# Kernel optimization log

Hardware: AMD Instinct MI355X
Metric: run time of the kernel (lower is better)

Reference implementation:

```python
import jax, jax.numpy as jnp
import numpy as np

K = 20            # top-k snippets selected per video
P = 0.1           # dropout prob applied to the selection mask
BATCH = 32        # number of normal videos (first half); abnormal is second half


def setup_inputs() -> dict:
    key = jax.random.key(0)
    k1, k2, k3, k4 = jax.random.split(key, 4)
    bs, t, f = 64, 2048, 1024
    features = jax.random.normal(k1, (bs, t, f), dtype=jnp.float32)
    scores = jax.random.uniform(k2, (bs, t, 1), dtype=jnp.float32)
    mask_u_abn = jax.random.uniform(k3, (BATCH, t), dtype=jnp.float32)
    mask_u_nor = jax.random.uniform(k4, (BATCH, t), dtype=jnp.float32)
    return {"features": features, "scores": scores,
            "mask_u_abn": mask_u_abn, "mask_u_nor": mask_u_nor}


def _select(feat, sc, mag, mask_u):
    # dropout on a ones tensor == Bernoulli(1-P) mask scaled by 1/(1-P)
    drop = (mask_u > P).astype(mag.dtype) / (1.0 - P)
    _, idx = jax.lax.top_k(mag * drop, K)            # [n, K] indices into t
    sel_feat = jnp.take_along_axis(feat, idx[:, :, None], axis=1)   # [n, K, f]
    sel_score = jnp.take_along_axis(sc, idx[:, :, None], axis=1)    # [n, K, 1]
    return jnp.mean(sel_score, axis=1), sel_feat     # [n,1], [n,K,f]


def reference(features, scores, mask_u_abn, mask_u_nor):
    # features: [bs, t, f], scores: [bs, t, 1]
    mags = jnp.linalg.norm(features, axis=2)         # [bs, t] L2 feature magnitudes
    nfeat, afeat = features[:BATCH], features[BATCH:]
    nsc, asc = scores[:BATCH], scores[BATCH:]
    nmag, amag = mags[:BATCH], mags[BATCH:]

    score_abnormal, abn_feamagnitude = _select(afeat, asc, amag, mask_u_abn)
    score_normal, nor_feamagnitude = _select(nfeat, nsc, nmag, mask_u_nor)
    return (score_abnormal, score_normal, abn_feamagnitude, nor_feamagnitude)
```

## Files before the change

### kernel.cpp

```cpp
#include <hip/hip_runtime.h>

#define T       2048
#define FEAT    1024
#define BTOT    64
#define BHALF   32
#define KSEL    20

__global__ __launch_bounds__(256) void mag_key_kernel(
        const float* __restrict__ feat,
        const float* __restrict__ mask_abn,
        const float* __restrict__ mask_nor,
        float* __restrict__ keys)
{
#pragma clang fp contract(off)
    const int wid  = threadIdx.x >> 6;
    const int lane = threadIdx.x & 63;
    const int row  = blockIdx.x * 4 + wid;

    __shared__ float sh[4 * 1056];
    float* lds = sh + wid * 1056;

    const float4* __restrict__ src = (const float4*)(feat + (size_t)row * FEAT);
#pragma unroll
    for (int it = 0; it < 4; ++it) {
        int f = it * 64 + lane;
        float4 v = src[f];
        int d = f * 4 + 4 * (f >> 5);
        *(float4*)(lds + d) = v;
    }
    __syncthreads();

    const int B = lane >> 3;
    const int j = lane & 7;
    const int base = B * 132 + j;

    float v0 = lds[base];
    float acc = v0 * v0;
#pragma unroll
    for (int i = 1; i < 16; ++i) {
        float w = lds[base + 8 * i];
        float p = w * w;
        acc = acc + p;
    }
    acc = acc + __shfl_xor(acc, 1);
    acc = acc + __shfl_xor(acc, 2);
    acc = acc + __shfl_xor(acc, 4);
    acc = acc + __shfl_xor(acc, 8);
    acc = acc + __shfl_xor(acc, 16);
    acc = acc + __shfl_xor(acc, 32);

    if (lane == 0) {
        float mag = sqrtf(acc);
        int b = row >> 11;
        int t = row & (T - 1);
        float m = (b < BHALF) ? mask_nor[b * T + t]
                              : mask_abn[(b - BHALF) * T + t];
        float key = (m > 0.1f) ? (mag * (1.0f / 0.9f)) : 0.0f;
        keys[row] = key;
    }
}

__global__ __launch_bounds__(256) void topk_kernel(
        const float* __restrict__ keys,
        const float* __restrict__ scores,
        int* __restrict__ sel_idx,
        float* __restrict__ out)
{
#pragma clang fp contract(off)
    const int b    = blockIdx.x;
    const int tid  = threadIdx.x;
    const int lane = tid & 63;
    const int wid  = tid >> 6;

    __shared__ unsigned long long wmax[2][4];
    __shared__ int s_sel[KSEL];

    unsigned long long p[8];
#pragma unroll
    for (int s = 0; s < 8; ++s) {
        int i = tid + 256 * s;
        float v = keys[b * T + i];
        p[s] = ((unsigned long long)__float_as_uint(v) << 32) |
               (unsigned long long)(0xFFFFFFFFu - (unsigned)i);
    }

    int sel_local[KSEL];

    for (int k = 0; k < KSEL; ++k) {
        unsigned long long best = 0ull;
#pragma unroll
        for (int s = 0; s < 8; ++s)
            if (p[s] > best) best = p[s];
#pragma unroll
        for (int d = 1; d < 64; d <<= 1) {
            unsigned long long o = __shfl_xor(best, d);
            if (o > best) best = o;
        }
        if (lane == 0) wmax[k & 1][wid] = best;
        __syncthreads();
        unsigned long long g = wmax[k & 1][0];
#pragma unroll
        for (int w = 1; w < 4; ++w)
            if (wmax[k & 1][w] > g) g = wmax[k & 1][w];
        int idx = (int)(0xFFFFFFFFu - (unsigned)(g & 0xFFFFFFFFull));
        sel_local[k] = idx;
        if ((idx & 255) == tid) p[idx >> 8] = 0ull;
    }

    if (tid == 0) {
        float a[KSEL];
        for (int k = 0; k < KSEL; ++k) a[k] = scores[b * T + sel_local[k]];
        float r[8];
        for (int jj = 0; jj < 8; ++jj) r[jj] = a[jj];
        for (int jj = 0; jj < 8; ++jj) r[jj] = r[jj] + a[8 + jj];
        float res = ((r[0] + r[1]) + (r[2] + r[3])) + ((r[4] + r[5]) + (r[6] + r[7]));
        res = res + a[16];
        res = res + a[17];
        res = res + a[18];
        res = res + a[19];
        float mean = res / 20.0f;
        int o = (b >= BHALF) ? (b - BHALF) : (BHALF + b);
        out[o] = mean;
    }
    if (tid < KSEL) sel_idx[b * KSEL + tid] = sel_local[tid];
}

__global__ __launch_bounds__(256) void gather_kernel(
        const float* __restrict__ feat,
        const int* __restrict__ sel_idx,
        float* __restrict__ out)
{
    const int k = blockIdx.x;
    const int b = blockIdx.y;
    const int t = sel_idx[b * KSEL + k];
    const float4* __restrict__ src =
        (const float4*)(feat + ((size_t)b * T + (size_t)t) * FEAT);
    size_t off;
    if (b >= BHALF) {
        off = 64 + ((size_t)(b - BHALF) * KSEL + k) * FEAT;
    } else {
        off = 64 + (size_t)BHALF * KSEL * FEAT + ((size_t)b * KSEL + k) * FEAT;
    }
    float4* __restrict__ dst = (float4*)(out + off);
    dst[threadIdx.x] = src[threadIdx.x];
}

extern "C" void kernel_launch(void* const* d_in, const int* in_sizes, int n_in,
                              void* d_out, int out_size, void* d_ws, size_t ws_size,
                              hipStream_t stream)
{
    const float* feat   = (const float*)d_in[0];
    const float* scores = (const float*)d_in[1];
    const float* mabn   = (const float*)d_in[2];
    const float* mnor   = (const float*)d_in[3];
    float* out = (float*)d_out;

    float* keys = (float*)d_ws;
    int*   sel  = (int*)((char*)d_ws + (size_t)BTOT * T * sizeof(float));

    mag_key_kernel<<<(BTOT * T) / 4, 256, 0, stream>>>(feat, mabn, mnor, keys);
    topk_kernel<<<BTOT, 256, 0, stream>>>(keys, scores, sel, out);
    gather_kernel<<<dim3(KSEL, BTOT), 256, 0, stream>>>(feat, sel, out);
}
```

Before: 686.4 us.

## Make magnitude kernel persistent with double-buffered direct global-to-LDS loads

```diff
diff --git a/kernel.cpp b/kernel.cpp
--- a/kernel.cpp
+++ b/kernel.cpp
@@ -5,64 +5,82 @@
 #define BTOT    64
 #define BHALF   32
 #define KSEL    20
+#define NROWS   (BTOT * T)
+#define MAG_BLOCKS 1280
+#define MAG_WAVES  (MAG_BLOCKS * 4)
 
-__global__ __launch_bounds__(256) void mag_key_kernel(
+__global__ __launch_bounds__(256) void mag_kernel(
         const float* __restrict__ feat,
-        const float* __restrict__ mask_abn,
-        const float* __restrict__ mask_nor,
         float* __restrict__ keys)
 {
 #pragma clang fp contract(off)
     const int wid  = threadIdx.x >> 6;
     const int lane = threadIdx.x & 63;
-    const int row  = blockIdx.x * 4 + wid;
+    const int gw   = blockIdx.x * 4 + wid;
 
-    __shared__ float sh[4 * 1056];
-    float* lds = sh + wid * 1056;
+    __shared__ float sh[4 * 2048];
+    float* buf = sh + wid * 2048;
 
-    const float4* __restrict__ src = (const float4*)(feat + (size_t)row * FEAT);
+    const int B    = lane >> 3;
+    const int j    = lane & 7;
+    const int base = B * 128 + j;
+    const int bl8  = lane & 24;
+
+    auto stage = [&](int row, float* dst) {
+        const float4* src4 = (const float4*)(feat + (size_t)row * FEAT);
 #pragma unroll
-    for (int it = 0; it < 4; ++it) {
-        int f = it * 64 + lane;
-        float4 v = src[f];
-        int d = f * 4 + 4 * (f >> 5);
-        *(float4*)(lds + d) = v;
-    }
-    __syncthreads();
+        for (int it = 0; it < 4; ++it) {
+            int q  = it * 64 + lane;
+            int qg = q ^ (((q >> 5) & 3) << 1);
+            __builtin_amdgcn_global_load_lds(
+                (const __attribute__((address_space(1))) void*)(src4 + qg),
+                (__attribute__((address_space(3))) void*)(dst + it * 256),
+                16, 0, 0);
+        }
+    };
 
-    const int B = lane >> 3;
-    const int j = lane & 7;
-    const int base = B * 132 + j;
+    int r = gw;
+    if (r < NROWS) stage(r, buf);
+    int cur = 0;
+    while (r < NROWS) {
+        const int rn = r + MAG_WAVES;
+        if (rn < NROWS) {
+            stage(rn, buf + ((cur ^ 1) << 10));
+            asm volatile("s_waitcnt vmcnt(4)" ::: "memory");
+        } else {
+            asm volatile("s_waitcnt vmcnt(0)" ::: "memory");
+        }
 
-    float v0 = lds[base];
-    float acc = v0 * v0;
+        const float* lds = buf + (cur << 10);
+
+        float w0  = lds[base + bl8];
+        float acc = w0 * w0;
 #pragma unroll
-    for (int i = 1; i < 16; ++i) {
-        float w = lds[base + 8 * i];
-        float p = w * w;
-        acc = acc + p;
-    }
-    acc = acc + __shfl_xor(acc, 1);
-    acc = acc + __shfl_xor(acc, 2);
-    acc = acc + __shfl_xor(acc, 4);
-    acc = acc + __shfl_xor(acc, 8);
-    acc = acc + __shfl_xor(acc, 16);
-    acc = acc + __shfl_xor(acc, 32);
+        for (int i = 1; i < 16; ++i) {
+            float w = lds[base + ((8 * i) ^ bl8)];
+            float p = w * w;
+            acc = acc + p;
+        }
+        acc = acc + __shfl_xor(acc, 1);
+        acc = acc + __shfl_xor(acc, 2);
+        acc = acc + __shfl_xor(acc, 4);
+        acc = acc + __shfl_xor(acc, 8);
+        acc = acc + __shfl_xor(acc, 16);
+        acc = acc + __shfl_xor(acc, 32);
 
-    if (lane == 0) {
-        float mag = sqrtf(acc);
-        int b = row >> 11;
-        int t = row & (T - 1);
-        float m = (b < BHALF) ? mask_nor[b * T + t]
-                              : mask_abn[(b - BHALF) * T + t];
-        float key = (m > 0.1f) ? (mag * (1.0f / 0.9f)) : 0.0f;
-        keys[row] = key;
+        if (lane == 0) keys[r] = sqrtf(acc);
+
+        asm volatile("s_waitcnt lgkmcnt(0)" ::: "memory");
+        cur ^= 1;
+        r = rn;
     }
 }
 
 __global__ __launch_bounds__(256) void topk_kernel(
         const float* __restrict__ keys,
         const float* __restrict__ scores,
+        const float* __restrict__ mask_abn,
+        const float* __restrict__ mask_nor,
         int* __restrict__ sel_idx,
         float* __restrict__ out)
 {
@@ -73,14 +91,16 @@
     const int wid  = tid >> 6;
 
     __shared__ unsigned long long wmax[2][4];
-    __shared__ int s_sel[KSEL];
 
     unsigned long long p[8];
 #pragma unroll
     for (int s = 0; s < 8; ++s) {
         int i = tid + 256 * s;
         float v = keys[b * T + i];
-        p[s] = ((unsigned long long)__float_as_uint(v) << 32) |
+        float m = (b < BHALF) ? mask_nor[b * T + i]
+                              : mask_abn[(b - BHALF) * T + i];
+        float key = (m > 0.1f) ? (v * (1.0f / 0.9f)) : 0.0f;
+        p[s] = ((unsigned long long)__float_as_uint(key) << 32) |
                (unsigned long long)(0xFFFFFFFFu - (unsigned)i);
     }
 
@@ -158,7 +178,7 @@
     float* keys = (float*)d_ws;
     int*   sel  = (int*)((char*)d_ws + (size_t)BTOT * T * sizeof(float));
 
-    mag_key_kernel<<<(BTOT * T) / 4, 256, 0, stream>>>(feat, mabn, mnor, keys);
-    topk_kernel<<<BTOT, 256, 0, stream>>>(keys, scores, sel, out);
+    mag_kernel<<<MAG_BLOCKS, 256, 0, stream>>>(feat, keys);
+    topk_kernel<<<BTOT, 256, 0, stream>>>(keys, scores, mabn, mnor, sel, out);
     gather_kernel<<<dim3(KSEL, BTOT), 256, 0, stream>>>(feat, sel, out);
 }
```

Measured after the change: 698.1 us. No clear change (+1.7%).
